# Performance work log

Hardware: AMD Instinct MI355X
Metric: run time of the kernel (lower is better)

## Reference

```python
import jax, jax.numpy as jnp
import numpy as np

B, D, T = 8, 256, 8192
N_Q, BINS = 8, 1024
COMMIT_W = 0.25

def setup_inputs() -> dict:
    key = jax.random.key(0)
    k1, k2 = jax.random.split(key)
    x = jax.random.normal(k1, (B, D, T), dtype=jnp.float32)
    codebooks = jax.random.normal(k2, (N_Q, BINS, D), dtype=jnp.float32)
    return {"x": x, "sample_rate": 16000, "codebooks": codebooks}

def _rvq(x_btd, codebooks):
    # x_btd: [B, T, D]; codebooks: [n_q, bins, D]
    def step(residual, cb):
        # nearest codebook entry under squared euclidean distance
        dots = jnp.einsum('btd,kd->btk', residual, cb)          # [B, T, K]
        cb_sq = jnp.sum(cb * cb, axis=-1)                        # [K]
        dist = cb_sq[None, None, :] - 2.0 * dots                 # argmin-equivalent distance
        idx = jnp.argmin(dist, axis=-1)                          # [B, T] int32
        q = cb[idx]                                              # [B, T, D] gather
        # commitment loss (codebook side detached, EnCodec style)
        loss = COMMIT_W * jnp.mean((jax.lax.stop_gradient(q) - residual) ** 2)
        # straight-through estimator
        q_ste = residual + jax.lax.stop_gradient(q - residual)
        return residual - q_ste, (q_ste, idx, loss)

    _, (qs, codes, losses) = jax.lax.scan(step, x_btd, codebooks)
    quantized = jnp.sum(qs, axis=0)                              # [B, T, D]
    return quantized, codes, losses

def reference(x, sample_rate, codebooks):
    n_q = codebooks.shape[0]
    bins = codebooks.shape[1]
    x_btd = jnp.transpose(x, (0, 2, 1))                          # [B, T, D]
    quantized_btd, codes, losses = _rvq(x_btd, codebooks)
    quantized = jnp.transpose(quantized_btd, (0, 2, 1))          # [B, D, T]
    bw_per_q = np.log2(bins) * sample_rate / 1000.0
    bw = jnp.asarray(n_q * bw_per_q, dtype=x.dtype)
    commit_loss = jnp.mean(losses)
    return quantized, codes, bw, commit_loss
```

## Files before the change

kernel.cpp:

```cpp
#include <hip/hip_runtime.h>
#include <math.h>

typedef _Float16 f16;
typedef f16 f16x8 __attribute__((ext_vector_type(8)));
typedef float f32x4 __attribute__((ext_vector_type(4)));

#define B_ 8
#define D_ 256
#define T_ 8192
#define NQ 8
#define KB 1024
#define TT 64
#define NTHR 512

#define OUT_CODES (B_ * D_ * T_)
#define OUT_BW (OUT_CODES + NQ * B_ * T_)
#define OUT_LOSS (OUT_BW + 1)

#define R_BYTES 65536
#define RED_OFF R_BYTES
#define REDI_OFF (RED_OFF + 1024)
#define WSUM_OFF (REDI_OFF + 1024)
#define LDS_TOTAL (WSUM_OFF + 32)

#define WS_HI (8192 * 4)
#define CBW_HALVES (NQ * 8 * KB * 32)
#define WS_LO (WS_HI + CBW_HALVES * 2)

__global__ void init_cbsq_kernel(const float* __restrict__ cb, const int* __restrict__ sr,
                                 float* __restrict__ csq, float* __restrict__ out) {
    int gid = blockIdx.x * blockDim.x + threadIdx.x;
    int row = gid >> 6;
    int lane = gid & 63;
    float4 v = ((const float4*)(cb + (size_t)row * D_))[lane];
    float s = fmaf(v.x, v.x, fmaf(v.y, v.y, fmaf(v.z, v.z, v.w * v.w)));
#pragma unroll
    for (int off = 32; off; off >>= 1) s += __shfl_down(s, off);
    if (lane == 0) csq[row] = s;
    if (gid == 0) {
        out[OUT_BW] = (float)(*sr) * (80.0f / 1000.0f);
        out[OUT_LOSS] = 0.0f;
    }
}

__global__ void init_split_kernel(const float* __restrict__ cb, f16* __restrict__ whi,
                                  f16* __restrict__ wlo) {
    int gid = blockIdx.x * 256 + threadIdx.x;
    int qdc = gid >> 10, k = gid & 1023;
    int q = qdc >> 3, dc = qdc & 7;
    const float* src = cb + ((size_t)(q * 1024 + k)) * 256 + dc * 32;
    size_t wo = (size_t)gid * 32;
#pragma unroll
    for (int jj = 0; jj < 4; ++jj) {
        float4 a = ((const float4*)src)[jj * 2];
        float4 c = ((const float4*)src)[jj * 2 + 1];
        float vals[8] = {a.x, a.y, a.z, a.w, c.x, c.y, c.z, c.w};
        f16x8 hv, lv;
#pragma unroll
        for (int i = 0; i < 8; ++i) {
            f16 h = (f16)vals[i];
            hv[i] = h;
            lv[i] = (f16)(vals[i] - (float)h);
        }
        *(f16x8*)&whi[wo + jj * 8] = hv;
        *(f16x8*)&wlo[wo + jj * 8] = lv;
    }
}

extern "C" __global__ __launch_bounds__(NTHR, 4)
void rvq_kernel(const float* __restrict__ x, const float* __restrict__ cb,
                const float* __restrict__ csq, const f16* __restrict__ whi,
                const f16* __restrict__ wlo, float* __restrict__ out) {
    extern __shared__ char smem[];
    f16* rs = (f16*)smem;
    float* redv = (float*)(smem + RED_OFF);
    int* redi = (int*)(smem + REDI_OFF);
    float* wsum = (float*)(smem + WSUM_OFF);

    const int tid = threadIdx.x;
    const int w = tid >> 6;
    const int l = tid & 63;
    const int l15 = l & 15;
    const int q4 = l >> 4;
    const int wm = w >> 2;
    const int wn = w & 3;

    const int b = blockIdx.x >> 7;
    const int t0 = (blockIdx.x & 127) * TT;
    const float* xb = x + (size_t)b * D_ * T_;

    for (int d = tid >> 6; d < D_; d += 8) {
        float v = xb[(size_t)d * T_ + t0 + l];
        f16 h = (f16)v;
        const int sw = l & 7;
        rs[l * 512 + (((d >> 3) ^ sw) << 3) + (d & 7)] = h;
        rs[l * 512 + ((((d >> 3) + 32) ^ sw) << 3) + (d & 7)] = (f16)(v - (float)h);
    }

    float ssq = 0.0f;

    for (int q = 0; q < NQ; ++q) {
        const float* cbq = cb + (size_t)q * KB * D_;
        const char* wq = (const char*)(whi + (size_t)q * 8 * KB * 32);
        const char* lq = (const char*)(wlo + (size_t)q * 8 * KB * 32);

        __syncthreads();

        float bval[8];
        int bidx[8];
#pragma unroll
        for (int e = 0; e < 8; ++e) { bval[e] = INFINITY; bidx[e] = 0; }

        const int swA = l15 & 7;

#pragma unroll 1
        for (int s = 0; s < 8; ++s) {
            const int code0 = s * 128 + wn * 32 + l15;
            const int vb0 = (code0 << 6) + q4 * 16;
            const int vb1 = vb0 + 1024;
            const float cq0 = csq[q * KB + code0];
            const float cq1 = csq[q * KB + code0 + 16];

            f32x4 ah[2][2];
#pragma unroll
            for (int mt = 0; mt < 2; ++mt)
#pragma unroll
                for (int nt = 0; nt < 2; ++nt) ah[mt][nt] = (f32x4)0.0f;

            f16x8 c0h = *(const f16x8*)(wq + vb0);
            f16x8 c0l = *(const f16x8*)(lq + vb0);
            f16x8 c1h = *(const f16x8*)(wq + vb1);
            f16x8 c1l = *(const f16x8*)(lq + vb1);

#pragma unroll 1
            for (int dc = 0; dc < 8; ++dc) {
                f16x8 n0h, n0l, n1h, n1l;
                if (dc < 7) {
                    const char* wd = wq + (dc + 1) * 65536;
                    const char* ld = lq + (dc + 1) * 65536;
                    n0h = *(const f16x8*)(wd + vb0);
                    n0l = *(const f16x8*)(ld + vb0);
                    n1h = *(const f16x8*)(wd + vb1);
                    n1l = *(const f16x8*)(ld + vb1);
                }
                const int ga = dc * 4 + q4;
                f16x8 af1[2], af2[2];
#pragma unroll
                for (int mt = 0; mt < 2; ++mt) {
                    const f16* rowp = rs + (wm * 32 + mt * 16 + l15) * 512;
                    af1[mt] = *(const f16x8*)&rowp[(ga ^ swA) << 3];
                    af2[mt] = *(const f16x8*)&rowp[((ga + 32) ^ swA) << 3];
                }
#pragma unroll
                for (int mt = 0; mt < 2; ++mt) {
                    ah[mt][0] = __builtin_amdgcn_mfma_f32_16x16x32_f16(af1[mt], c0h, ah[mt][0], 0, 0, 0);
                    ah[mt][0] = __builtin_amdgcn_mfma_f32_16x16x32_f16(af2[mt], c0h, ah[mt][0], 0, 0, 0);
                    ah[mt][0] = __builtin_amdgcn_mfma_f32_16x16x32_f16(af1[mt], c0l, ah[mt][0], 0, 0, 0);
                    ah[mt][1] = __builtin_amdgcn_mfma_f32_16x16x32_f16(af1[mt], c1h, ah[mt][1], 0, 0, 0);
                    ah[mt][1] = __builtin_amdgcn_mfma_f32_16x16x32_f16(af2[mt], c1h, ah[mt][1], 0, 0, 0);
                    ah[mt][1] = __builtin_amdgcn_mfma_f32_16x16x32_f16(af1[mt], c1l, ah[mt][1], 0, 0, 0);
                }
                if (dc < 7) { c0h = n0h; c0l = n0l; c1h = n1h; c1l = n1l; }
            }
#pragma unroll
            for (int nt = 0; nt < 2; ++nt) {
                const int code = code0 + nt * 16;
                const float cq = nt ? cq1 : cq0;
#pragma unroll
                for (int mt = 0; mt < 2; ++mt)
#pragma unroll
                    for (int rg = 0; rg < 4; ++rg) {
                        const float dist = fmaf(-2.0f, ah[mt][nt][rg], cq);
                        const int e = mt * 4 + rg;
                        if (dist < bval[e]) { bval[e] = dist; bidx[e] = code; }
                    }
            }
        }
#pragma unroll
        for (int m = 1; m < 16; m <<= 1) {
#pragma unroll
            for (int e = 0; e < 8; ++e) {
                const float ov = __shfl_xor(bval[e], m);
                const int oi = __shfl_xor(bidx[e], m);
                if (ov < bval[e] || (ov == bval[e] && oi < bidx[e])) { bval[e] = ov; bidx[e] = oi; }
            }
        }
        if (l15 == 0) {
#pragma unroll
            for (int mt = 0; mt < 2; ++mt)
#pragma unroll
                for (int rg = 0; rg < 4; ++rg) {
                    const int tl = mt * 16 + q4 * 4 + rg;
                    redv[w * 32 + tl] = bval[mt * 4 + rg];
                    redi[w * 32 + tl] = bidx[mt * 4 + rg];
                }
        }
        __syncthreads();
        {
            const int t = tid & 63, ch = tid >> 6;
            const int wmr = t >> 5, tl = t & 31;
            float bv = redv[(wmr * 4) * 32 + tl];
            int bi = redi[(wmr * 4) * 32 + tl];
#pragma unroll
            for (int w2 = 1; w2 < 4; ++w2) {
                const float v = redv[(wmr * 4 + w2) * 32 + tl];
                const int ii = redi[(wmr * 4 + w2) * 32 + tl];
                if (v < bv || (v == bv && ii < bi)) { bv = v; bi = ii; }
            }
            if (ch == 0) out[OUT_CODES + ((size_t)q * B_ + b) * T_ + t0 + t] = (float)bi;
            const float* crow = cbq + (size_t)bi * D_ + ch * 32;
            f16* rowp = rs + t * 512;
            const int sw = t & 7;
#pragma unroll
            for (int jj = 0; jj < 4; ++jj) {
                const int g = ch * 4 + jj;
                const int g1 = (g ^ sw) << 3;
                const int g2 = ((g + 32) ^ sw) << 3;
                f16x8 hv = *(const f16x8*)&rowp[g1];
                f16x8 lv = *(const f16x8*)&rowp[g2];
                const float4 c0 = ((const float4*)crow)[jj * 2];
                const float4 c1 = ((const float4*)crow)[jj * 2 + 1];
                const float cc[8] = {c0.x, c0.y, c0.z, c0.w, c1.x, c1.y, c1.z, c1.w};
                f16x8 nh, nl;
#pragma unroll
                for (int i = 0; i < 8; ++i) {
                    const float r = (float)hv[i] + (float)lv[i];
                    const float nv = r - cc[i];
                    ssq = fmaf(nv, nv, ssq);
                    const f16 h = (f16)nv;
                    nh[i] = h;
                    nl[i] = (f16)(nv - (float)h);
                }
                *(f16x8*)&rowp[g1] = nh;
                *(f16x8*)&rowp[g2] = nl;
            }
        }
    }
    __syncthreads();
    {
        float* outq = out + (size_t)b * D_ * T_;
        for (int d = tid >> 6; d < D_; d += 8) {
            const int sw = l & 7;
            const float h1 = (float)rs[l * 512 + (((d >> 3) ^ sw) << 3) + (d & 7)];
            const float h2 = (float)rs[l * 512 + ((((d >> 3) + 32) ^ sw) << 3) + (d & 7)];
            const size_t gi = (size_t)d * T_ + t0 + l;
            outq[gi] = xb[gi] - (h1 + h2);
        }
    }
#pragma unroll
    for (int off = 32; off; off >>= 1) ssq += __shfl_down(ssq, off);
    if (l == 0) wsum[w] = ssq;
    __syncthreads();
    if (tid == 0) {
        float tot = 0.0f;
#pragma unroll
        for (int i = 0; i < 8; ++i) tot += wsum[i];
        const float scale = 0.25f / ((float)NQ * (float)B_ * (float)D_ * (float)T_);
        atomicAdd(out + OUT_LOSS, tot * scale);
    }
}

extern "C" void kernel_launch(void* const* d_in, const int* in_sizes, int n_in,
                              void* d_out, int out_size, void* d_ws, size_t ws_size,
                              hipStream_t stream) {
    const float* x = (const float*)d_in[0];
    const int* sr = (const int*)d_in[1];
    const float* cb = (const float*)d_in[2];
    float* out = (float*)d_out;
    float* csq = (float*)d_ws;
    f16* whi = (f16*)((char*)d_ws + WS_HI);
    f16* wlo = (f16*)((char*)d_ws + WS_LO);

    hipFuncSetAttribute((const void*)rvq_kernel, hipFuncAttributeMaxDynamicSharedMemorySize,
                        LDS_TOTAL);

    init_cbsq_kernel<<<2048, 256, 0, stream>>>(cb, sr, csq, out);
    init_split_kernel<<<256, 256, 0, stream>>>(cb, whi, wlo);
    rvq_kernel<<<B_ * (T_ / TT), NTHR, LDS_TOTAL, stream>>>(x, cb, csq, whi, wlo, out);
}
```

Measured before the change: 1.150 ms.

## Give each wave all 64 rows with 32 codes to halve codebook reloads

Changes the wave-to-tile mapping. Each of the 8 waves now covers all 64 time rows against its own 32 codes per step, so codebook fragments are loaded from global memory half as often. The MFMA chain is interleaved with LDS loads of the next row group using sched_barrier, and best indices are packed two per 32-bit register to offset the doubled accumulator and best-value state. The cross-wave reduction now spans 8 waves, and register pressure rises, which may hurt occupancy under the launch bounds of 4 blocks per CU.

```diff
diff --git a/kernel.cpp b/kernel.cpp
--- a/kernel.cpp
+++ b/kernel.cpp
@@ -19,13 +19,15 @@
 
 #define R_BYTES 65536
 #define RED_OFF R_BYTES
-#define REDI_OFF (RED_OFF + 1024)
-#define WSUM_OFF (REDI_OFF + 1024)
+#define REDI_OFF (RED_OFF + 2048)
+#define WSUM_OFF (REDI_OFF + 2048)
 #define LDS_TOTAL (WSUM_OFF + 32)
 
 #define WS_HI (8192 * 4)
 #define CBW_HALVES (NQ * 8 * KB * 32)
 #define WS_LO (WS_HI + CBW_HALVES * 2)
+
+#define MFMA16(a, b, c) __builtin_amdgcn_mfma_f32_16x16x32_f16(a, b, c, 0, 0, 0)
 
 __global__ void init_cbsq_kernel(const float* __restrict__ cb, const int* __restrict__ sr,
                                  float* __restrict__ csq, float* __restrict__ out) {
@@ -82,8 +84,6 @@
     const int l = tid & 63;
     const int l15 = l & 15;
     const int q4 = l >> 4;
-    const int wm = w >> 2;
-    const int wn = w & 3;
 
     const int b = blockIdx.x >> 7;
     const int t0 = (blockIdx.x & 127) * TT;
@@ -106,31 +106,30 @@
 
         __syncthreads();
 
-        float bval[8];
-        int bidx[8];
-#pragma unroll
-        for (int e = 0; e < 8; ++e) { bval[e] = INFINITY; bidx[e] = 0; }
+        float bval[16];
+        unsigned bidxp[8];
+#pragma unroll
+        for (int e = 0; e < 16; ++e) bval[e] = INFINITY;
+#pragma unroll
+        for (int p = 0; p < 8; ++p) bidxp[p] = 0;
 
         const int swA = l15 & 7;
 
 #pragma unroll 1
-        for (int s = 0; s < 8; ++s) {
-            const int code0 = s * 128 + wn * 32 + l15;
+        for (int s = 0; s < 4; ++s) {
+            const int code0 = s * 256 + w * 32 + l15;
             const int vb0 = (code0 << 6) + q4 * 16;
-            const int vb1 = vb0 + 1024;
-            const float cq0 = csq[q * KB + code0];
-            const float cq1 = csq[q * KB + code0 + 16];
-
-            f32x4 ah[2][2];
-#pragma unroll
-            for (int mt = 0; mt < 2; ++mt)
+
+            f32x4 ah[4][2];
+#pragma unroll
+            for (int mt = 0; mt < 4; ++mt)
 #pragma unroll
                 for (int nt = 0; nt < 2; ++nt) ah[mt][nt] = (f32x4)0.0f;
 
             f16x8 c0h = *(const f16x8*)(wq + vb0);
             f16x8 c0l = *(const f16x8*)(lq + vb0);
-            f16x8 c1h = *(const f16x8*)(wq + vb1);
-            f16x8 c1l = *(const f16x8*)(lq + vb1);
+            f16x8 c1h = *(const f16x8*)(wq + vb0 + 1024);
+            f16x8 c1l = *(const f16x8*)(lq + vb0 + 1024);
 
 #pragma unroll 1
             for (int dc = 0; dc < 8; ++dc) {
@@ -140,71 +139,115 @@
                     const char* ld = lq + (dc + 1) * 65536;
                     n0h = *(const f16x8*)(wd + vb0);
                     n0l = *(const f16x8*)(ld + vb0);
-                    n1h = *(const f16x8*)(wd + vb1);
-                    n1l = *(const f16x8*)(ld + vb1);
+                    n1h = *(const f16x8*)(wd + vb0 + 1024);
+                    n1l = *(const f16x8*)(ld + vb0 + 1024);
                 }
                 const int ga = dc * 4 + q4;
-                f16x8 af1[2], af2[2];
-#pragma unroll
-                for (int mt = 0; mt < 2; ++mt) {
-                    const f16* rowp = rs + (wm * 32 + mt * 16 + l15) * 512;
-                    af1[mt] = *(const f16x8*)&rowp[(ga ^ swA) << 3];
-                    af2[mt] = *(const f16x8*)&rowp[((ga + 32) ^ swA) << 3];
-                }
-#pragma unroll
-                for (int mt = 0; mt < 2; ++mt) {
-                    ah[mt][0] = __builtin_amdgcn_mfma_f32_16x16x32_f16(af1[mt], c0h, ah[mt][0], 0, 0, 0);
-                    ah[mt][0] = __builtin_amdgcn_mfma_f32_16x16x32_f16(af2[mt], c0h, ah[mt][0], 0, 0, 0);
-                    ah[mt][0] = __builtin_amdgcn_mfma_f32_16x16x32_f16(af1[mt], c0l, ah[mt][0], 0, 0, 0);
-                    ah[mt][1] = __builtin_amdgcn_mfma_f32_16x16x32_f16(af1[mt], c1h, ah[mt][1], 0, 0, 0);
-                    ah[mt][1] = __builtin_amdgcn_mfma_f32_16x16x32_f16(af2[mt], c1h, ah[mt][1], 0, 0, 0);
-                    ah[mt][1] = __builtin_amdgcn_mfma_f32_16x16x32_f16(af1[mt], c1l, ah[mt][1], 0, 0, 0);
-                }
+                const int o1 = (ga ^ swA) << 3;
+                const int o2 = ((ga + 32) ^ swA) << 3;
+
+                const f16* r0 = rs + (0 * 16 + l15) * 512;
+                f16x8 afa1 = *(const f16x8*)&r0[o1];
+                f16x8 afa2 = *(const f16x8*)&r0[o2];
+                const f16* r1 = rs + (1 * 16 + l15) * 512;
+                f16x8 afb1 = *(const f16x8*)&r1[o1];
+                f16x8 afb2 = *(const f16x8*)&r1[o2];
+                ah[0][0] = MFMA16(afa1, c0h, ah[0][0]);
+                ah[0][0] = MFMA16(afa2, c0h, ah[0][0]);
+                ah[0][0] = MFMA16(afa1, c0l, ah[0][0]);
+                ah[0][1] = MFMA16(afa1, c1h, ah[0][1]);
+                ah[0][1] = MFMA16(afa2, c1h, ah[0][1]);
+                ah[0][1] = MFMA16(afa1, c1l, ah[0][1]);
+                __builtin_amdgcn_sched_barrier(0);
+                const f16* r2 = rs + (2 * 16 + l15) * 512;
+                afa1 = *(const f16x8*)&r2[o1];
+                afa2 = *(const f16x8*)&r2[o2];
+                ah[1][0] = MFMA16(afb1, c0h, ah[1][0]);
+                ah[1][0] = MFMA16(afb2, c0h, ah[1][0]);
+                ah[1][0] = MFMA16(afb1, c0l, ah[1][0]);
+                ah[1][1] = MFMA16(afb1, c1h, ah[1][1]);
+                ah[1][1] = MFMA16(afb2, c1h, ah[1][1]);
+                ah[1][1] = MFMA16(afb1, c1l, ah[1][1]);
+                __builtin_amdgcn_sched_barrier(0);
+                const f16* r3 = rs + (3 * 16 + l15) * 512;
+                afb1 = *(const f16x8*)&r3[o1];
+                afb2 = *(const f16x8*)&r3[o2];
+                ah[2][0] = MFMA16(afa1, c0h, ah[2][0]);
+                ah[2][0] = MFMA16(afa2, c0h, ah[2][0]);
+                ah[2][0] = MFMA16(afa1, c0l, ah[2][0]);
+                ah[2][1] = MFMA16(afa1, c1h, ah[2][1]);
+                ah[2][1] = MFMA16(afa2, c1h, ah[2][1]);
+                ah[2][1] = MFMA16(afa1, c1l, ah[2][1]);
+                __builtin_amdgcn_sched_barrier(0);
+                ah[3][0] = MFMA16(afb1, c0h, ah[3][0]);
+                ah[3][0] = MFMA16(afb2, c0h, ah[3][0]);
+                ah[3][0] = MFMA16(afb1, c0l, ah[3][0]);
+                ah[3][1] = MFMA16(afb1, c1h, ah[3][1]);
+                ah[3][1] = MFMA16(afb2, c1h, ah[3][1]);
+                ah[3][1] = MFMA16(afb1, c1l, ah[3][1]);
+                __builtin_amdgcn_sched_barrier(0);
                 if (dc < 7) { c0h = n0h; c0l = n0l; c1h = n1h; c1l = n1l; }
             }
+            const float cq0 = csq[q * KB + code0];
+            const float cq1 = csq[q * KB + code0 + 16];
 #pragma unroll
             for (int nt = 0; nt < 2; ++nt) {
                 const int code = code0 + nt * 16;
                 const float cq = nt ? cq1 : cq0;
 #pragma unroll
-                for (int mt = 0; mt < 2; ++mt)
+                for (int mt = 0; mt < 4; ++mt)
 #pragma unroll
                     for (int rg = 0; rg < 4; ++rg) {
+                        const int e = mt * 4 + rg;
                         const float dist = fmaf(-2.0f, ah[mt][nt][rg], cq);
-                        const int e = mt * 4 + rg;
-                        if (dist < bval[e]) { bval[e] = dist; bidx[e] = code; }
+                        if (dist < bval[e]) {
+                            bval[e] = dist;
+                            const int sh = (e & 1) * 16;
+                            bidxp[e >> 1] = (bidxp[e >> 1] & ~(0xFFFFu << sh)) |
+                                            ((unsigned)code << sh);
+                        }
                     }
             }
         }
 #pragma unroll
         for (int m = 1; m < 16; m <<= 1) {
 #pragma unroll
-            for (int e = 0; e < 8; ++e) {
-                const float ov = __shfl_xor(bval[e], m);
-                const int oi = __shfl_xor(bidx[e], m);
-                if (ov < bval[e] || (ov == bval[e] && oi < bidx[e])) { bval[e] = ov; bidx[e] = oi; }
+            for (int p = 0; p < 8; ++p) {
+                const unsigned op = __shfl_xor((int)bidxp[p], m);
+#pragma unroll
+                for (int h = 0; h < 2; ++h) {
+                    const int e = p * 2 + h;
+                    const float ov = __shfl_xor(bval[e], m);
+                    const int sh = h * 16;
+                    const unsigned oc = (op >> sh) & 0xFFFFu;
+                    const unsigned mc = (bidxp[p] >> sh) & 0xFFFFu;
+                    if (ov < bval[e] || (ov == bval[e] && oc < mc)) {
+                        bval[e] = ov;
+                        bidxp[p] = (bidxp[p] & ~(0xFFFFu << sh)) | (oc << sh);
+                    }
+                }
             }
         }
         if (l15 == 0) {
 #pragma unroll
-            for (int mt = 0; mt < 2; ++mt)
+            for (int mt = 0; mt < 4; ++mt)
 #pragma unroll
                 for (int rg = 0; rg < 4; ++rg) {
-                    const int tl = mt * 16 + q4 * 4 + rg;
-                    redv[w * 32 + tl] = bval[mt * 4 + rg];
-                    redi[w * 32 + tl] = bidx[mt * 4 + rg];
+                    const int e = mt * 4 + rg;
+                    const int t = mt * 16 + q4 * 4 + rg;
+                    redv[w * 64 + t] = bval[e];
+                    redi[w * 64 + t] = (int)((bidxp[e >> 1] >> ((e & 1) * 16)) & 0xFFFFu);
                 }
         }
         __syncthreads();
         {
             const int t = tid & 63, ch = tid >> 6;
-            const int wmr = t >> 5, tl = t & 31;
-            float bv = redv[(wmr * 4) * 32 + tl];
-            int bi = redi[(wmr * 4) * 32 + tl];
-#pragma unroll
-            for (int w2 = 1; w2 < 4; ++w2) {
-                const float v = redv[(wmr * 4 + w2) * 32 + tl];
-                const int ii = redi[(wmr * 4 + w2) * 32 + tl];
+            float bv = redv[t];
+            int bi = redi[t];
+#pragma unroll
+            for (int w2 = 1; w2 < 8; ++w2) {
+                const float v = redv[w2 * 64 + t];
+                const int ii = redi[w2 * 64 + t];
                 if (v < bv || (v == bv && ii < bi)) { bv = v; bi = ii; }
             }
             if (ch == 0) out[OUT_CODES + ((size_t)q * B_ + b) * T_ + t0 + t] = (float)bi;
```

Result: faster. 1.018 ms (-11.5%).
